# Performance work log

Hardware: AMD Instinct MI355X
Metric: run time of the kernel (lower is better)

Reference implementation:

```python
import jax, jax.numpy as jnp
import numpy as np

N_WORDS = 30000
EMB_DIM = 784  # 28*28
MAT_DIM = 28
BATCH = 1024
SEQ_LEN = 64


def setup_inputs() -> dict:
    key = jax.random.key(0)
    k_sent, k_tab = jax.random.split(key)
    # token ids in [0, n_words]; row 0 is the neutral (identity) / padding element
    sent = jax.random.randint(k_sent, (BATCH, SEQ_LEN), 0, N_WORDS + 1, dtype=jnp.int32).astype(jnp.int64)
    eye_flat = jnp.eye(MAT_DIM, dtype=jnp.float32).reshape(-1)
    # 'identity' init strategy: identity + small gaussian noise (scale kept small for stability of long products)
    table = eye_flat + 0.01 * jax.random.normal(k_tab, (N_WORDS + 1, EMB_DIM), dtype=jnp.float32)
    table = table.at[0].set(eye_flat)  # neutral element at padding_idx=0
    return {"sent": sent, "table": table}


def reference(sent, table):
    # sent: [B, S] int ids; table: [n_words+1, d*d]
    B, S = sent.shape
    d = MAT_DIM
    word_mats = table[sent].reshape(B, S, d, d)  # embedding lookup + unflatten
    # CMOW: continual multiplication cur = cur @ W_i, sequential over seq dim
    init = word_mats[:, 0]                      # [B, d, d]
    rest = jnp.moveaxis(word_mats[:, 1:], 1, 0)  # [S-1, B, d, d]

    def step(cur, w):
        return jnp.matmul(cur, w), None

    cur, _ = jax.lax.scan(step, init, rest)
    return cur.reshape(B, d * d)  # flatten matrix back to embedding
```

## Files before the change

### kernel.cpp

```cpp
#include <hip/hip_runtime.h>
#include <stdint.h>

#define SEQ 64
#define D 28
#define EMB 784
#define CH 8
#define BUFF 832
#define CTW 36
#define CTSZ (32 * CTW)

typedef float float4v __attribute__((ext_vector_type(4)));
typedef __bf16 bf16x8 __attribute__((ext_vector_type(8)));

union FragU { unsigned u[4]; bf16x8 v; };

__device__ __forceinline__ unsigned fbits(float x) { union { float f; unsigned u; } t; t.f = x; return t.u; }
__device__ __forceinline__ float fof(unsigned u) { union { unsigned u; float f; } t; t.u = u; return t.f; }

__device__ __forceinline__ void split_frags(const float x[8], bf16x8& hi, bf16x8& lo)
{
    FragU H, L;
#pragma unroll
    for (int p = 0; p < 4; ++p) {
        unsigned ua = fbits(x[2 * p]), ub = fbits(x[2 * p + 1]);
        H.u[p] = (ua >> 16) | (ub & 0xFFFF0000u);
        unsigned la = fbits(x[2 * p]     - fof(ua & 0xFFFF0000u));
        unsigned lb = fbits(x[2 * p + 1] - fof(ub & 0xFFFF0000u));
        L.u[p] = (la >> 16) | (lb & 0xFFFF0000u);
    }
    hi = H.v; lo = L.v;
}

__device__ __forceinline__ void dma_row(const float* grow, float* lbuf, int lane)
{
    const char* g16 = (const char*)grow + lane * 16;
    const char* g4  = (const char*)grow + 3072 + lane * 4;
    char* l = (char*)lbuf;
    __builtin_amdgcn_global_load_lds((const __attribute__((address_space(1))) void*)(g16),
                                     (__attribute__((address_space(3))) void*)(l), 16, 0, 0);
    __builtin_amdgcn_global_load_lds((const __attribute__((address_space(1))) void*)(g16 + 1024),
                                     (__attribute__((address_space(3))) void*)(l + 1024), 16, 0, 0);
    __builtin_amdgcn_global_load_lds((const __attribute__((address_space(1))) void*)(g16 + 2048),
                                     (__attribute__((address_space(3))) void*)(l + 2048), 16, 0, 0);
    __builtin_amdgcn_global_load_lds((const __attribute__((address_space(1))) void*)(g4),
                                     (__attribute__((address_space(3))) void*)(l + 3072), 4, 0, 0);
}

template <int CNT, typename F>
__device__ __forceinline__ void mfma_chain(F rowptr,
                                           float* __restrict__ CTw,
                                           float* __restrict__ B0,
                                           float* __restrict__ B1,
                                           float4v acc[2][2],
                                           int lane)
{
    const int c = lane & 15;
    const int quad = lane >> 4;
    const bool q3 = (quad == 3);

    dma_row(rowptr(0), B0, lane);
    dma_row(rowptr(1), B1, lane);
    __builtin_amdgcn_s_waitcnt(0x0074);

#pragma unroll
    for (int R = 0; R < 2; ++R)
#pragma unroll
        for (int Cc = 0; Cc < 2; ++Cc)
#pragma unroll
            for (int i = 0; i < 4; ++i) {
                const int rr = 16 * R + 4 * quad + i;
                const int cc = 16 * Cc + c;
                acc[R][Cc][i] = B0[(rr < D ? rr : D - 1) * D + (cc < D ? cc : D - 1)];
            }
    __builtin_amdgcn_s_waitcnt(0xC07F);

#pragma unroll 1
    for (int j = 1; j < CNT; ++j) {
        const int jn = (j + 1 < CNT) ? (j + 1) : j;
        float* nB = (j & 1) ? B0 : B1;
        float* cB = (j & 1) ? B1 : B0;
        dma_row(rowptr(jn), nB, lane);

#pragma unroll
        for (int R = 0; R < 2; ++R)
#pragma unroll
            for (int Cc = 0; Cc < 2; ++Cc)
#pragma unroll
                for (int i = 0; i < 4; ++i)
                    CTw[(16 * R + 4 * quad + i) * CTW + 16 * Cc + c] = acc[R][Cc][i];

        __builtin_amdgcn_sched_barrier(0);
        __builtin_amdgcn_s_waitcnt(0x0074);
        __builtin_amdgcn_sched_barrier(0);

        bf16x8 Ah[2], Al[2];
#pragma unroll
        for (int R = 0; R < 2; ++R) {
            const float* ap = CTw + (16 * R + c) * CTW + 8 * quad;
            float4v x0 = *(const float4v*)ap;
            float4v x1 = *(const float4v*)(ap + 4);
            if (q3) x1 = float4v{0.f, 0.f, 0.f, 0.f};
            float x[8] = {x0.x, x0.y, x0.z, x0.w, x1.x, x1.y, x1.z, x1.w};
            split_frags(x, Ah[R], Al[R]);
        }

        bf16x8 Bh[2], Bl[2];
#pragma unroll
        for (int Cc = 0; Cc < 2; ++Cc) {
            const float* bp = cB + (8 * quad) * D + 16 * Cc + c;
            float x[8];
#pragma unroll
            for (int t = 0; t < 8; ++t) x[t] = bp[t * D];
            if (q3) { x[4] = 0.f; x[5] = 0.f; x[6] = 0.f; x[7] = 0.f; }
            split_frags(x, Bh[Cc], Bl[Cc]);
        }

#pragma unroll
        for (int R = 0; R < 2; ++R)
#pragma unroll
            for (int Cc = 0; Cc < 2; ++Cc) {
                float4v d = {0.f, 0.f, 0.f, 0.f};
                d = __builtin_amdgcn_mfma_f32_16x16x32_bf16(Ah[R], Bh[Cc], d, 0, 0, 0);
                d = __builtin_amdgcn_mfma_f32_16x16x32_bf16(Ah[R], Bl[Cc], d, 0, 0, 0);
                d = __builtin_amdgcn_mfma_f32_16x16x32_bf16(Al[R], Bh[Cc], d, 0, 0, 0);
                acc[R][Cc] = d;
            }
    }
}

__device__ __forceinline__ void store_acc(const float4v acc[2][2],
                                          float* __restrict__ orow, int lane)
{
    const int c = lane & 15;
    const int quad = lane >> 4;
#pragma unroll
    for (int R = 0; R < 2; ++R)
#pragma unroll
        for (int Cc = 0; Cc < 2; ++Cc)
#pragma unroll
            for (int i = 0; i < 4; ++i) {
                const int row = 16 * R + 4 * quad + i;
                const int col = 16 * Cc + c;
                if (row < D && col < D) orow[row * D + col] = acc[R][Cc][i];
            }
}

__global__ __launch_bounds__(128, 1) void w2m_leaf_mfma(
    const int* __restrict__ sent,
    const float* __restrict__ table,
    float* __restrict__ ws0)
{
    __shared__ float CT[2 * CTSZ] __attribute__((aligned(16)));
    __shared__ float BB[2 * 2 * BUFF] __attribute__((aligned(16)));
    const int lane = threadIdx.x & 63;
    const int wid  = threadIdx.x >> 6;
    const int w = blockIdx.x * 2 + wid;
    const int b = w >> 3;
    const int g = w & 7;
    float* CTw = &CT[wid * CTSZ];
    float* B0 = &BB[wid * 2 * BUFF];
    float* B1 = B0 + BUFF;

    const int myidx = sent[b * SEQ + 8 * g + (lane & 7)];
    int jl[CH];
#pragma unroll
    for (int j = 0; j < CH; ++j) jl[j] = __builtin_amdgcn_readlane(myidx, j);

    float4v acc[2][2];
    mfma_chain<CH>([&](int j) { return table + (size_t)jl[j] * EMB; },
                   CTw, B0, B1, acc, lane);

    store_acc(acc, ws0 + (size_t)w * EMB, lane);
}

__global__ __launch_bounds__(128, 1) void w2m_top_mfma(
    const float* __restrict__ ws0,
    float* __restrict__ out)
{
    __shared__ float CT[2 * CTSZ] __attribute__((aligned(16)));
    __shared__ float BB[2 * 2 * BUFF] __attribute__((aligned(16)));
    const int lane = threadIdx.x & 63;
    const int wid  = threadIdx.x >> 6;
    const int b = blockIdx.x * 2 + wid;
    float* CTw = &CT[wid * CTSZ];
    float* B0 = &BB[wid * 2 * BUFF];
    float* B1 = B0 + BUFF;

    const float* base = ws0 + (size_t)b * CH * EMB;
    float4v acc[2][2];
    mfma_chain<CH>([&](int j) { return base + (size_t)j * EMB; },
                   CTw, B0, B1, acc, lane);

    store_acc(acc, out + (size_t)b * EMB, lane);
}

__device__ __forceinline__ void xpose_write(const float4v ct[4],
                                            float* __restrict__ LTw,
                                            int it, int jt)
{
#pragma unroll
    for (int cc = 0; cc < 4; ++cc) {
        float4v t;
        t.x = ct[0][cc]; t.y = ct[1][cc]; t.z = ct[2][cc]; t.w = ct[3][cc];
        *(float4v*)&LTw[(4 * jt + cc) * D + 4 * it] = t;
    }
}

__global__ __launch_bounds__(64, 1) void w2m_serial(
    const int* __restrict__ sent,
    const float* __restrict__ table,
    float* __restrict__ out)
{
    __shared__ float LT[EMB] __attribute__((aligned(16)));
    __shared__ float BBs[2 * BUFF] __attribute__((aligned(16)));
    const int lane = threadIdx.x;
    const int b = blockIdx.x;
    int it = lane / 7, jt = lane % 7;
    const bool act = lane < 49;
    if (!act) { it = 6; jt = 6; }

    const int myidx = sent[b * SEQ + lane];
    int jls[SEQ];
#pragma unroll
    for (int s = 0; s < SEQ; ++s) jls[s] = __builtin_amdgcn_readlane(myidx, s);

    const float* row0 = table + (size_t)jls[0] * EMB;
    float4v ct[4];
#pragma unroll
    for (int r = 0; r < 4; ++r)
        ct[r] = *(const float4v*)(row0 + (4 * it + r) * D + 4 * jt);

    float* Bs0 = &BBs[0];
    float* Bs1 = &BBs[BUFF];
    dma_row(table + (size_t)jls[1] * EMB, Bs1, lane);

#pragma unroll 1
    for (int j = 1; j < SEQ; ++j) {
        const int jn = (j + 1 < SEQ) ? (j + 1) : j;
        float* nB = (j & 1) ? Bs0 : Bs1;
        float* cB = (j & 1) ? Bs1 : Bs0;
        dma_row(table + (size_t)jls[jn] * EMB, nB, lane);

        xpose_write(ct, LT, it, jt);

        __builtin_amdgcn_sched_barrier(0);
        __builtin_amdgcn_s_waitcnt(0x0074);
        __builtin_amdgcn_sched_barrier(0);

        const float* ap = LT + 4 * it;
        const float* bp = cB + 4 * jt;
        float4v acc[4] = {};
#pragma unroll
        for (int k = 0; k < 28; ++k) {
            float4v av = *(const float4v*)(ap + k * D);
            float4v bb = *(const float4v*)(bp + k * D);
#pragma unroll
            for (int r = 0; r < 4; ++r) acc[r] += bb * av[r];
        }
#pragma unroll
        for (int r = 0; r < 4; ++r) ct[r] = acc[r];
    }

    if (act) {
        float* orow = out + (size_t)b * EMB;
#pragma unroll
        for (int r = 0; r < 4; ++r)
            *(float4v*)(orow + (4 * it + r) * D + 4 * jt) = ct[r];
    }
}

extern "C" void kernel_launch(void* const* d_in, const int* in_sizes, int n_in,
                              void* d_out, int out_size, void* d_ws, size_t ws_size,
                              hipStream_t stream) {
    const int* sent = (const int*)d_in[0];
    const float* table = (const float*)d_in[1];
    float* out = (float*)d_out;
    const int batch = in_sizes[0] / SEQ;
    const size_t ws_needed = (size_t)batch * CH * EMB * sizeof(float);

    if (ws_size >= ws_needed) {
        float* ws0 = (float*)d_ws;
        const int waves1 = batch * CH;
        hipLaunchKernelGGL(w2m_leaf_mfma, dim3(waves1 / 2), dim3(128), 0, stream,
                           sent, table, ws0);
        hipLaunchKernelGGL(w2m_top_mfma, dim3(batch / 2), dim3(128), 0, stream,
                           ws0, out);
    } else {
        hipLaunchKernelGGL(w2m_serial, dim3(batch), dim3(64), 0, stream,
                           sent, table, out);
    }
}
```

Measured before the change: 163.0 us.

## Fuse two-level chain product into one kernel with LDS wave reduction

Replaces the leaf and top kernels with a single kernel: each block handles one batch row with four waves, each multiplying a 16-matrix segment. The partial products are combined in shared memory, replacing the workspace round-trip and second launch. It also drops the serial fallback path. The trade-off is fewer waves in flight and a longer serial chain per wave, with the combine step done redundantly by all waves.

```diff
diff --git a/kernel.cpp b/kernel.cpp
--- a/kernel.cpp
+++ b/kernel.cpp
@@ -4,7 +4,8 @@
 #define SEQ 64
 #define D 28
 #define EMB 784
-#define CH 8
+#define NW 4
+#define CH 16
 #define BUFF 832
 #define CTW 36
 #define CTSZ (32 * CTW)
@@ -46,6 +47,67 @@
                                      (__attribute__((address_space(3))) void*)(l + 3072), 4, 0, 0);
 }
 
+
+__device__ __forceinline__ void publish_C(const float4v acc[2][2], float* dst, int lane)
+{
+    const int c = lane & 15;
+    const int quad = lane >> 4;
+#pragma unroll
+    for (int R = 0; R < 2; ++R)
+#pragma unroll
+        for (int Cc = 0; Cc < 2; ++Cc)
+#pragma unroll
+            for (int i = 0; i < 4; ++i)
+                dst[(16 * R + 4 * quad + i) * CTW + 16 * Cc + c] = acc[R][Cc][i];
+}
+
+__device__ __forceinline__ void load_A(const float* ct, int lane, bf16x8 Ah[2], bf16x8 Al[2])
+{
+    const int c = lane & 15;
+    const int quad = lane >> 4;
+    const bool q3 = (quad == 3);
+#pragma unroll
+    for (int R = 0; R < 2; ++R) {
+        const float* ap = ct + (16 * R + c) * CTW + 8 * quad;
+        float4v x0 = *(const float4v*)ap;
+        float4v x1 = *(const float4v*)(ap + 4);
+        if (q3) x1 = float4v{0.f, 0.f, 0.f, 0.f};
+        float x[8] = {x0.x, x0.y, x0.z, x0.w, x1.x, x1.y, x1.z, x1.w};
+        split_frags(x, Ah[R], Al[R]);
+    }
+}
+
+__device__ __forceinline__ void load_B(const float* buf, int stride, int lane, bf16x8 Bh[2], bf16x8 Bl[2])
+{
+    const int c = lane & 15;
+    const int quad = lane >> 4;
+    const bool q3 = (quad == 3);
+#pragma unroll
+    for (int Cc = 0; Cc < 2; ++Cc) {
+        const float* bp = buf + (8 * quad) * stride + 16 * Cc + c;
+        float x[8];
+#pragma unroll
+        for (int t = 0; t < 8; ++t) x[t] = bp[t * stride];
+        if (q3) { x[4] = 0.f; x[5] = 0.f; x[6] = 0.f; x[7] = 0.f; }
+        split_frags(x, Bh[Cc], Bl[Cc]);
+    }
+}
+
+__device__ __forceinline__ void mm_step(float4v acc[2][2], const bf16x8 Ah[2], const bf16x8 Al[2],
+                                        const bf16x8 Bh[2], const bf16x8 Bl[2])
+{
+#pragma unroll
+    for (int R = 0; R < 2; ++R)
+#pragma unroll
+        for (int Cc = 0; Cc < 2; ++Cc) {
+            float4v d = {0.f, 0.f, 0.f, 0.f};
+            d = __builtin_amdgcn_mfma_f32_16x16x32_bf16(Ah[R], Bh[Cc], d, 0, 0, 0);
+            d = __builtin_amdgcn_mfma_f32_16x16x32_bf16(Ah[R], Bl[Cc], d, 0, 0, 0);
+            d = __builtin_amdgcn_mfma_f32_16x16x32_bf16(Al[R], Bh[Cc], d, 0, 0, 0);
+            acc[R][Cc] = d;
+        }
+}
+
 template <int CNT, typename F>
 __device__ __forceinline__ void mfma_chain(F rowptr,
                                            float* __restrict__ CTw,
@@ -56,7 +118,6 @@
 {
     const int c = lane & 15;
     const int quad = lane >> 4;
-    const bool q3 = (quad == 3);
 
     dma_row(rowptr(0), B0, lane);
     dma_row(rowptr(1), B1, lane);
@@ -81,50 +142,16 @@
         float* cB = (j & 1) ? B1 : B0;
         dma_row(rowptr(jn), nB, lane);
 
-#pragma unroll
-        for (int R = 0; R < 2; ++R)
-#pragma unroll
-            for (int Cc = 0; Cc < 2; ++Cc)
-#pragma unroll
-                for (int i = 0; i < 4; ++i)
-                    CTw[(16 * R + 4 * quad + i) * CTW + 16 * Cc + c] = acc[R][Cc][i];
+        publish_C(acc, CTw, lane);
 
         __builtin_amdgcn_sched_barrier(0);
         __builtin_amdgcn_s_waitcnt(0x0074);
         __builtin_amdgcn_sched_barrier(0);
 
-        bf16x8 Ah[2], Al[2];
-#pragma unroll
-        for (int R = 0; R < 2; ++R) {
-            const float* ap = CTw + (16 * R + c) * CTW + 8 * quad;
-            float4v x0 = *(const float4v*)ap;
-            float4v x1 = *(const float4v*)(ap + 4);
-            if (q3) x1 = float4v{0.f, 0.f, 0.f, 0.f};
-            float x[8] = {x0.x, x0.y, x0.z, x0.w, x1.x, x1.y, x1.z, x1.w};
-            split_frags(x, Ah[R], Al[R]);
-        }
-
-        bf16x8 Bh[2], Bl[2];
-#pragma unroll
-        for (int Cc = 0; Cc < 2; ++Cc) {
-            const float* bp = cB + (8 * quad) * D + 16 * Cc + c;
-            float x[8];
-#pragma unroll
-            for (int t = 0; t < 8; ++t) x[t] = bp[t * D];
-            if (q3) { x[4] = 0.f; x[5] = 0.f; x[6] = 0.f; x[7] = 0.f; }
-            split_frags(x, Bh[Cc], Bl[Cc]);
-        }
-
-#pragma unroll
-        for (int R = 0; R < 2; ++R)
-#pragma unroll
-            for (int Cc = 0; Cc < 2; ++Cc) {
-                float4v d = {0.f, 0.f, 0.f, 0.f};
-                d = __builtin_amdgcn_mfma_f32_16x16x32_bf16(Ah[R], Bh[Cc], d, 0, 0, 0);
-                d = __builtin_amdgcn_mfma_f32_16x16x32_bf16(Ah[R], Bl[Cc], d, 0, 0, 0);
-                d = __builtin_amdgcn_mfma_f32_16x16x32_bf16(Al[R], Bh[Cc], d, 0, 0, 0);
-                acc[R][Cc] = d;
-            }
+        bf16x8 Ah[2], Al[2], Bh[2], Bl[2];
+        load_A(CTw, lane, Ah, Al);
+        load_B(cB, D, lane, Bh, Bl);
+        mm_step(acc, Ah, Al, Bh, Bl);
     }
 }
 
@@ -145,23 +172,21 @@
             }
 }
 
-__global__ __launch_bounds__(128, 1) void w2m_leaf_mfma(
+__global__ __launch_bounds__(NW * 64, 1) void w2m_fused(
     const int* __restrict__ sent,
     const float* __restrict__ table,
-    float* __restrict__ ws0)
-{
-    __shared__ float CT[2 * CTSZ] __attribute__((aligned(16)));
-    __shared__ float BB[2 * 2 * BUFF] __attribute__((aligned(16)));
+    float* __restrict__ out)
+{
+    __shared__ float SH[NW * CTSZ + NW * 2 * BUFF] __attribute__((aligned(16)));
     const int lane = threadIdx.x & 63;
     const int wid  = threadIdx.x >> 6;
-    const int w = blockIdx.x * 2 + wid;
-    const int b = w >> 3;
-    const int g = w & 7;
-    float* CTw = &CT[wid * CTSZ];
-    float* B0 = &BB[wid * 2 * BUFF];
-    float* B1 = B0 + BUFF;
-
-    const int myidx = sent[b * SEQ + 8 * g + (lane & 7)];
+    const int b = blockIdx.x;
+
+    float* CTw = &SH[wid * CTSZ];
+    float* B0  = &SH[NW * CTSZ + wid * 2 * BUFF];
+    float* B1  = B0 + BUFF;
+
+    const int myidx = sent[b * SEQ + CH * wid + (lane & (CH - 1))];
     int jl[CH];
 #pragma unroll
     for (int j = 0; j < CH; ++j) jl[j] = __builtin_amdgcn_readlane(myidx, j);
@@ -170,103 +195,33 @@
     mfma_chain<CH>([&](int j) { return table + (size_t)jl[j] * EMB; },
                    CTw, B0, B1, acc, lane);
 
-    store_acc(acc, ws0 + (size_t)w * EMB, lane);
-}
-
-__global__ __launch_bounds__(128, 1) void w2m_top_mfma(
-    const float* __restrict__ ws0,
-    float* __restrict__ out)
-{
-    __shared__ float CT[2 * CTSZ] __attribute__((aligned(16)));
-    __shared__ float BB[2 * 2 * BUFF] __attribute__((aligned(16)));
-    const int lane = threadIdx.x & 63;
-    const int wid  = threadIdx.x >> 6;
-    const int b = blockIdx.x * 2 + wid;
-    float* CTw = &CT[wid * CTSZ];
-    float* B0 = &BB[wid * 2 * BUFF];
-    float* B1 = B0 + BUFF;
-
-    const float* base = ws0 + (size_t)b * CH * EMB;
-    float4v acc[2][2];
-    mfma_chain<CH>([&](int j) { return base + (size_t)j * EMB; },
-                   CTw, B0, B1, acc, lane);
-
-    store_acc(acc, out + (size_t)b * EMB, lane);
-}
-
-__device__ __forceinline__ void xpose_write(const float4v ct[4],
-                                            float* __restrict__ LTw,
-                                            int it, int jt)
-{
-#pragma unroll
-    for (int cc = 0; cc < 4; ++cc) {
-        float4v t;
-        t.x = ct[0][cc]; t.y = ct[1][cc]; t.z = ct[2][cc]; t.w = ct[3][cc];
-        *(float4v*)&LTw[(4 * jt + cc) * D + 4 * it] = t;
-    }
-}
-
-__global__ __launch_bounds__(64, 1) void w2m_serial(
-    const int* __restrict__ sent,
-    const float* __restrict__ table,
-    float* __restrict__ out)
-{
-    __shared__ float LT[EMB] __attribute__((aligned(16)));
-    __shared__ float BBs[2 * BUFF] __attribute__((aligned(16)));
-    const int lane = threadIdx.x;
-    const int b = blockIdx.x;
-    int it = lane / 7, jt = lane % 7;
-    const bool act = lane < 49;
-    if (!act) { it = 6; jt = 6; }
-
-    const int myidx = sent[b * SEQ + lane];
-    int jls[SEQ];
-#pragma unroll
-    for (int s = 0; s < SEQ; ++s) jls[s] = __builtin_amdgcn_readlane(myidx, s);
-
-    const float* row0 = table + (size_t)jls[0] * EMB;
-    float4v ct[4];
-#pragma unroll
-    for (int r = 0; r < 4; ++r)
-        ct[r] = *(const float4v*)(row0 + (4 * it + r) * D + 4 * jt);
-
-    float* Bs0 = &BBs[0];
-    float* Bs1 = &BBs[BUFF];
-    dma_row(table + (size_t)jls[1] * EMB, Bs1, lane);
-
+    publish_C(acc, CTw, lane);
+    __syncthreads();
+
+    const int c = lane & 15;
+    const int quad = lane >> 4;
+#pragma unroll
+    for (int R = 0; R < 2; ++R)
+#pragma unroll
+        for (int Cc = 0; Cc < 2; ++Cc)
+#pragma unroll
+            for (int i = 0; i < 4; ++i)
+                acc[R][Cc][i] = SH[(16 * R + 4 * quad + i) * CTW + 16 * Cc + c];
+
+    float* Sw = B0;
 #pragma unroll 1
-    for (int j = 1; j < SEQ; ++j) {
-        const int jn = (j + 1 < SEQ) ? (j + 1) : j;
-        float* nB = (j & 1) ? Bs0 : Bs1;
-        float* cB = (j & 1) ? Bs1 : Bs0;
-        dma_row(table + (size_t)jls[jn] * EMB, nB, lane);
-
-        xpose_write(ct, LT, it, jt);
-
-        __builtin_amdgcn_sched_barrier(0);
-        __builtin_amdgcn_s_waitcnt(0x0074);
-        __builtin_amdgcn_sched_barrier(0);
-
-        const float* ap = LT + 4 * it;
-        const float* bp = cB + 4 * jt;
-        float4v acc[4] = {};
-#pragma unroll
-        for (int k = 0; k < 28; ++k) {
-            float4v av = *(const float4v*)(ap + k * D);
-            float4v bb = *(const float4v*)(bp + k * D);
-#pragma unroll
-            for (int r = 0; r < 4; ++r) acc[r] += bb * av[r];
-        }
-#pragma unroll
-        for (int r = 0; r < 4; ++r) ct[r] = acc[r];
-    }
-
-    if (act) {
-        float* orow = out + (size_t)b * EMB;
-#pragma unroll
-        for (int r = 0; r < 4; ++r)
-            *(float4v*)(orow + (4 * it + r) * D + 4 * jt) = ct[r];
-    }
+    for (int j = 1; j < NW; ++j) {
+        publish_C(acc, Sw, lane);
+        __builtin_amdgcn_sched_barrier(0);
+        __builtin_amdgcn_s_waitcnt(0xC07F);
+        __builtin_amdgcn_sched_barrier(0);
+        bf16x8 Ah[2], Al[2], Bh[2], Bl[2];
+        load_A(Sw, lane, Ah, Al);
+        load_B(&SH[j * CTSZ], CTW, lane, Bh, Bl);
+        mm_step(acc, Ah, Al, Bh, Bl);
+    }
+
+    if (wid == 0) store_acc(acc, out + (size_t)b * EMB, lane);
 }
 
 extern "C" void kernel_launch(void* const* d_in, const int* in_sizes, int n_in,
@@ -276,17 +231,8 @@
     const float* table = (const float*)d_in[1];
     float* out = (float*)d_out;
     const int batch = in_sizes[0] / SEQ;
-    const size_t ws_needed = (size_t)batch * CH * EMB * sizeof(float);
-
-    if (ws_size >= ws_needed) {
-        float* ws0 = (float*)d_ws;
-        const int waves1 = batch * CH;
-        hipLaunchKernelGGL(w2m_leaf_mfma, dim3(waves1 / 2), dim3(128), 0, stream,
-                           sent, table, ws0);
-        hipLaunchKernelGGL(w2m_top_mfma, dim3(batch / 2), dim3(128), 0, stream,
-                           ws0, out);
-    } else {
-        hipLaunchKernelGGL(w2m_serial, dim3(batch), dim3(64), 0, stream,
-                           sent, table, out);
-    }
-}
+    (void)d_ws; (void)ws_size;
+
+    hipLaunchKernelGGL(w2m_fused, dim3(batch), dim3(NW * 64), 0, stream,
+                       sent, table, out);
+}
```

Result: faster. 157.3 us (-3.5%).
